# Performance work log

Hardware: AMD Instinct MI355X
Metric: run time of the kernel (lower is better)

The kernel has to match this reference:

```python
import jax, jax.numpy as jnp
import numpy as np

DIM = 1024
HEADS = 16
HEAD_DIM = DIM // HEADS
ROPE_BASE = 500000.0
SCALE = HEAD_DIM ** -0.5


def _rope_cos_sin(T, dtype=jnp.float32):
    inv_freq = 1.0 / (ROPE_BASE ** (jnp.arange(0, HEAD_DIM, 2, dtype=jnp.float32) / HEAD_DIM))
    t = jnp.arange(T, dtype=jnp.float32)
    freqs = t[:, None] * inv_freq[None, :]            # (T, hd/2)
    emb = jnp.concatenate([freqs, freqs], axis=-1)    # (T, hd)
    return jnp.cos(emb).astype(dtype), jnp.sin(emb).astype(dtype)


def _rotate_half(x):
    x1, x2 = jnp.split(x, 2, axis=-1)
    return jnp.concatenate([-x2, x1], axis=-1)


def _apply_rope(x, cos, sin):
    # x: (B,H,T,hd); cos/sin: (T,hd)
    return x * cos + _rotate_half(x) * sin


def setup_inputs() -> dict:
    key = jax.random.key(0)
    k1, k2, k3 = jax.random.split(key, 3)
    B, T = 4, 4096
    x = jax.random.normal(k1, (B, T, DIM), dtype=jnp.float32)
    W_qkv = jax.random.normal(k2, (DIM, 3 * DIM), dtype=jnp.float32) * (DIM ** -0.5)
    W_out = jax.random.normal(k3, (DIM, DIM), dtype=jnp.float32) * (DIM ** -0.5)
    return {"x": x, "W_qkv": W_qkv, "W_out": W_out}


def reference(x, W_qkv, W_out):
    B, T, D = x.shape
    H, hd = HEADS, HEAD_DIM
    qkv = (x @ W_qkv).reshape(B, T, 3, H, hd).transpose(2, 0, 3, 1, 4)  # (3,B,H,T,hd)
    q, k, v = qkv[0], qkv[1], qkv[2]
    cos, sin = _rope_cos_sin(T, q.dtype)
    q = _apply_rope(q, cos, sin)
    k = _apply_rope(k, cos, sin)
    # linear attention: elu+1 feature map
    q_feat = jax.nn.elu(q * SCALE) + 1.0
    k_feat = jax.nn.elu(k) + 1.0
    kv = jnp.einsum('bhtd,bhtv->bhdv', k_feat, v)      # (B,H,hd,hd)
    k_sum = k_feat.sum(axis=2)                          # (B,H,hd)
    denom = jnp.maximum(jnp.einsum('bhtd,bhd->bht', q_feat, k_sum), 1e-6)
    out = jnp.einsum('bhtd,bhdv->bhtv', q_feat, kv) / denom[..., None]
    out = out.transpose(0, 2, 1, 3).reshape(B, T, D)
    return out @ W_out
```

## Files before the change

### kernel.cpp

```cpp
#include <hip/hip_runtime.h>
#include <hip/hip_bf16.h>

typedef __bf16 bf16;
typedef bf16 bf16x4 __attribute__((ext_vector_type(4)));
typedef bf16 bf16x8 __attribute__((ext_vector_type(8)));
typedef float f32x4 __attribute__((ext_vector_type(4)));

#define GLD_LDS16(gptr, lptr) \
  __builtin_amdgcn_global_load_lds((const __attribute__((address_space(1))) unsigned int*)(gptr), \
                                   (__attribute__((address_space(3))) unsigned int*)(lptr), 16, 0, 0)

__global__ __launch_bounds__(256) void f32_to_bf16(const float* __restrict__ in,
                                                   bf16* __restrict__ out) {
  const size_t i = ((size_t)blockIdx.x * 256 + threadIdx.x) * 8;
  float4 a = *(const float4*)(in + i);
  float4 b = *(const float4*)(in + i + 4);
  bf16x8 o;
  o[0] = (bf16)a.x; o[1] = (bf16)a.y; o[2] = (bf16)a.z; o[3] = (bf16)a.w;
  o[4] = (bf16)b.x; o[5] = (bf16)b.y; o[6] = (bf16)b.z; o[7] = (bf16)b.w;
  *(bf16x8*)(out + i) = o;
}

__global__ __launch_bounds__(256) void transpose_f32_bf16(const float* __restrict__ in,
                                                          bf16* __restrict__ out,
                                                          int R, int C) {
  __shared__ float tile[32][33];
  const int bx = blockIdx.x * 32;
  const int by = blockIdx.y * 32;
  const int tx = threadIdx.x & 31;
  const int ty = threadIdx.x >> 5;
#pragma unroll
  for (int i = 0; i < 4; i++) {
    int r = by + ty + i * 8;
    tile[ty + i * 8][tx] = in[(size_t)r * C + bx + tx];
  }
  __syncthreads();
#pragma unroll
  for (int i = 0; i < 4; i++) {
    int r = bx + ty + i * 8;
    out[(size_t)r * R + by + tx] = (bf16)tile[tx][ty + i * 8];
  }
}

__device__ __forceinline__ void gemm_core(const bf16* __restrict__ A,
                                          const bf16* __restrict__ BT,
                                          int K, int m0, int n0,
                                          bf16* As, bf16* Bs,
                                          f32x4 acc[4][4]) {
  const int tid = threadIdx.x;
  const int lane = tid & 63;
  const int wave = tid >> 6;
  const int wm = wave & 1, wn = wave >> 1;

#pragma unroll
  for (int i = 0; i < 4; i++)
#pragma unroll
    for (int j = 0; j < 4; j++) acc[i][j] = f32x4{0.f, 0.f, 0.f, 0.f};

  const int srow = lane >> 3;
  const int pch = lane & 7;
  const int scol = (pch ^ srow) * 8;
  const int rbase = wave * 32;

  const bf16* Ag = A + (size_t)(m0 + rbase + srow) * K + scol;
  const bf16* Bg = BT + (size_t)(n0 + rbase + srow) * K + scol;
  bf16* Al = As + rbase * 64;
  bf16* Bl = Bs + rbase * 64;

  for (int k0 = 0; k0 < K; k0 += 64) {
#pragma unroll
    for (int i = 0; i < 4; i++) {
      GLD_LDS16(Ag + (size_t)i * 8 * K + k0, Al + i * 512);
      GLD_LDS16(Bg + (size_t)i * 8 * K + k0, Bl + i * 512);
    }
    __syncthreads();
    const int fr = lane & 15;
    const int sw = fr & 7;
#pragma unroll
    for (int kk = 0; kk < 64; kk += 32) {
      const int lc = (kk >> 3) + (lane >> 4);
      const int pc8 = (lc ^ sw) * 8;
      bf16x8 af[4], bfv[4];
#pragma unroll
      for (int mi = 0; mi < 4; mi++)
        af[mi] = *(const bf16x8*)(As + (wm * 64 + mi * 16 + fr) * 64 + pc8);
#pragma unroll
      for (int ni = 0; ni < 4; ni++)
        bfv[ni] = *(const bf16x8*)(Bs + (wn * 64 + ni * 16 + fr) * 64 + pc8);
#pragma unroll
      for (int mi = 0; mi < 4; mi++)
#pragma unroll
        for (int ni = 0; ni < 4; ni++)
          acc[mi][ni] = __builtin_amdgcn_mfma_f32_16x16x32_bf16(af[mi], bfv[ni], acc[mi][ni], 0, 0, 0);
    }
    __syncthreads();
  }
}

__global__ __launch_bounds__(256) void gemm_qkv_fused(const bf16* __restrict__ A,
                                                      const bf16* __restrict__ BT,
                                                      bf16* __restrict__ qfB,
                                                      bf16* __restrict__ kfB,
                                                      bf16* __restrict__ vfB) {
  __shared__ __attribute__((aligned(16))) bf16 As[128 * 64];
  __shared__ __attribute__((aligned(16))) bf16 Bs[128 * 64];
  const int K = 1024;
  const int m0 = blockIdx.y * 128, n0 = blockIdx.x * 128;

  f32x4 acc[4][4];
  gemm_core(A, BT, K, m0, n0, As, Bs, acc);

  const int lane = threadIdx.x & 63;
  const int wave = threadIdx.x >> 6;
  const int wm = wave & 1, wn = wave >> 1;
  const int cb = n0 + wn * 64;
  const int p = cb >> 10;
  const int hh = (cb & 1023) >> 6;
  const int fr15 = lane & 15;
  const int row00 = m0 + wm * 64 + ((lane >> 4) << 2);
  const int b = row00 >> 12;
  const size_t base0 = ((size_t)(b * 16 + hh)) * 4096 * 64;

  if (p == 2) {
#pragma unroll
    for (int mi = 0; mi < 4; mi++)
#pragma unroll
      for (int r = 0; r < 4; r++) {
        const int tloc = (row00 + mi * 16 + r) & 4095;
        bf16* dst = vfB + base0 + (size_t)tloc * 64;
#pragma unroll
        for (int ni = 0; ni < 4; ni++) dst[fr15 + ni * 16] = (bf16)acc[mi][ni][r];
      }
  } else {
    bf16* outp = (p == 0) ? qfB : kfB;
    const float scl = (p == 0) ? 0.125f : 1.0f;
    const float invf0 = (float)exp(-((double)fr15 / 32.0) * log(500000.0));
    const float invf1 = (float)exp(-((double)(fr15 + 16) / 32.0) * log(500000.0));
#pragma unroll
    for (int mi = 0; mi < 4; mi++)
#pragma unroll
      for (int r = 0; r < 4; r++) {
        const int tloc = (row00 + mi * 16 + r) & 4095;
        const float tf = (float)tloc;
        bf16* dst = outp + base0 + (size_t)tloc * 64;
#pragma unroll
        for (int ni = 0; ni < 2; ni++) {
          float x1 = acc[mi][ni][r], x2 = acc[mi][ni + 2][r];
          float sn, cs;
          sincosf(tf * (ni ? invf1 : invf0), &sn, &cs);
          float r1 = (x1 * cs - x2 * sn) * scl;
          float r2 = (x2 * cs + x1 * sn) * scl;
          dst[fr15 + ni * 16] = (bf16)(r1 > 0.f ? r1 + 1.f : __expf(r1));
          dst[fr15 + ni * 16 + 32] = (bf16)(r2 > 0.f ? r2 + 1.f : __expf(r2));
        }
      }
  }
}

__global__ __launch_bounds__(256) void gemm_bt_f32(const bf16* __restrict__ A,
                                                   const bf16* __restrict__ BT,
                                                   float* __restrict__ C,
                                                   int N, int K) {
  __shared__ __attribute__((aligned(16))) bf16 As[128 * 64];
  __shared__ __attribute__((aligned(16))) bf16 Bs[128 * 64];
  const int m0 = blockIdx.y * 128, n0 = blockIdx.x * 128;

  f32x4 acc[4][4];
  gemm_core(A, BT, K, m0, n0, As, Bs, acc);

  const int lane = threadIdx.x & 63;
  const int wave = threadIdx.x >> 6;
  const int wm = wave & 1, wn = wave >> 1;
  const int col0 = n0 + wn * 64 + (lane & 15);
  const int row00 = m0 + wm * 64 + ((lane >> 4) << 2);
#pragma unroll
  for (int mi = 0; mi < 4; mi++)
#pragma unroll
    for (int ni = 0; ni < 4; ni++)
#pragma unroll
      for (int r = 0; r < 4; r++)
        C[(size_t)(row00 + mi * 16 + r) * N + col0 + ni * 16] = acc[mi][ni][r];
}

__global__ __launch_bounds__(256) void attn_kv(const bf16* __restrict__ kfB,
                                               const bf16* __restrict__ vfB,
                                               float* __restrict__ kvg,
                                               float* __restrict__ ksumg) {
  const int bh = blockIdx.x;
  const int t0 = blockIdx.y * 256;
  __shared__ __attribute__((aligned(16))) float kfs[32][68];
  __shared__ __attribute__((aligned(16))) float vfs[32][68];
  const int tid = threadIdx.x;
  const int dq = tid & 15, g = tid >> 4;
  const int tl = tid >> 3, ch = (tid & 7) * 8;

  f32x4 acc[4];
#pragma unroll
  for (int r = 0; r < 4; r++) acc[r] = f32x4{0.f, 0.f, 0.f, 0.f};
  float ksa[4] = {0.f, 0.f, 0.f, 0.f};

  for (int sc = 0; sc < 8; sc++) {
    const size_t rowb = ((size_t)bh * 4096 + t0 + sc * 32 + tl) * 64 + ch;
    bf16x8 k8 = *(const bf16x8*)(kfB + rowb);
    bf16x8 v8 = *(const bf16x8*)(vfB + rowb);
    f32x4 ka, kb, va, vb;
#pragma unroll
    for (int j = 0; j < 4; j++) {
      ka[j] = (float)k8[j]; kb[j] = (float)k8[j + 4];
      va[j] = (float)v8[j]; vb[j] = (float)v8[j + 4];
    }
    *(f32x4*)&kfs[tl][ch] = ka;
    *(f32x4*)&kfs[tl][ch + 4] = kb;
    *(f32x4*)&vfs[tl][ch] = va;
    *(f32x4*)&vfs[tl][ch + 4] = vb;
    __syncthreads();

#pragma unroll 8
    for (int t = 0; t < 32; t++) {
      f32x4 kq = *(const f32x4*)&kfs[t][dq * 4];
      f32x4 vq = *(const f32x4*)&vfs[t][g * 4];
#pragma unroll
      for (int r = 0; r < 4; r++) {
#pragma unroll
        for (int c = 0; c < 4; c++) acc[r][c] += kq[r] * vq[c];
      }
      if (g == 0) {
#pragma unroll
        for (int r = 0; r < 4; r++) ksa[r] += kq[r];
      }
    }
    __syncthreads();
  }

#pragma unroll
  for (int r = 0; r < 4; r++)
#pragma unroll
    for (int c = 0; c < 4; c++)
      atomicAdd(&kvg[(size_t)bh * 4096 + (dq * 4 + r) * 64 + g * 4 + c], acc[r][c]);
  if (g == 0) {
#pragma unroll
    for (int r = 0; r < 4; r++) atomicAdd(&ksumg[bh * 64 + dq * 4 + r], ksa[r]);
  }
}

__global__ __launch_bounds__(256) void attn_out(const bf16* __restrict__ qfB,
                                                const float* __restrict__ kvg,
                                                const float* __restrict__ ksumg,
                                                bf16* __restrict__ attn) {
  const int bh = blockIdx.y;
  const int b = bh >> 4, h = bh & 15;
  const int t0 = blockIdx.x * 64;
  __shared__ __attribute__((aligned(16))) float qf[64][68];
  __shared__ __attribute__((aligned(16))) float kvs[64][64];
  __shared__ __attribute__((aligned(16))) float ksums[64];
  const int tid = threadIdx.x;

#pragma unroll
  for (int j = 0; j < 2; j++) {
    int chunk = tid + 256 * j;
    int tl = chunk >> 3, col = (chunk & 7) * 8;
    bf16x8 r = *(const bf16x8*)(qfB + ((size_t)bh * 4096 + t0 + tl) * 64 + col);
    f32x4 a, bb;
#pragma unroll
    for (int q = 0; q < 4; q++) { a[q] = (float)r[q]; bb[q] = (float)r[q + 4]; }
    *(f32x4*)&qf[tl][col] = a;
    *(f32x4*)&qf[tl][col + 4] = bb;
  }
#pragma unroll
  for (int j = 0; j < 4; j++) {
    int idx = tid + 256 * j;
    *(float4*)&kvs[idx >> 4][(idx & 15) * 4] = *(const float4*)&kvg[(size_t)bh * 4096 + idx * 4];
  }
  if (tid < 64) ksums[tid] = ksumg[bh * 64 + tid];
  __syncthreads();

  const int tr = tid >> 4, cc = tid & 15;
  f32x4 acc[4];
#pragma unroll
  for (int r = 0; r < 4; r++) acc[r] = f32x4{0.f, 0.f, 0.f, 0.f};
  f32x4 dn = f32x4{0.f, 0.f, 0.f, 0.f};

  for (int d2 = 0; d2 < 64; d2++) {
    f32x4 kv4 = *(const f32x4*)&kvs[d2][cc * 4];
    float ks = ksums[d2];
#pragma unroll
    for (int r = 0; r < 4; r++) {
      float qv = qf[tr * 4 + r][d2];
      acc[r] += qv * kv4;
      dn[r] += qv * ks;
    }
  }

#pragma unroll
  for (int r = 0; r < 4; r++) {
    const float rdn = 1.f / fmaxf(dn[r], 1e-6f);
    bf16x4 o;
#pragma unroll
    for (int c = 0; c < 4; c++) o[c] = (bf16)(acc[r][c] * rdn);
    *(bf16x4*)(attn + ((size_t)(b * 4096) + t0 + tr * 4 + r) * 1024 + h * 64 + cc * 4) = o;
  }
}

extern "C" void kernel_launch(void* const* d_in, const int* in_sizes, int n_in,
                              void* d_out, int out_size, void* d_ws, size_t ws_size,
                              hipStream_t stream) {
  if (ws_size < 177225728ULL) return;

  const float* x = (const float*)d_in[0];
  const float* Wqkv = (const float*)d_in[1];
  const float* Wout = (const float*)d_in[2];
  float* out = (float*)d_out;
  char* ws = (char*)d_ws;

  float* kvg = (float*)(ws);
  float* ksumg = (float*)(ws + 1048576);
  bf16* WqkvT = (bf16*)(ws + 1064960);
  bf16* WoutT = (bf16*)(ws + 7356416);
  bf16* attn = (bf16*)(ws + 9453568);
  bf16* qfB = (bf16*)(ws + 43008000);
  bf16* kfB = (bf16*)(ws + 76562432);
  bf16* vfB = (bf16*)(ws + 110116864);
  bf16* xB = (bf16*)(ws + 143671296);

  hipMemsetAsync(ws, 0, 1048576 + 16384, stream);

  f32_to_bf16<<<16777216 / (256 * 8), 256, 0, stream>>>(x, xB);
  transpose_f32_bf16<<<dim3(3072 / 32, 1024 / 32), 256, 0, stream>>>(Wqkv, WqkvT, 1024, 3072);
  transpose_f32_bf16<<<dim3(1024 / 32, 1024 / 32), 256, 0, stream>>>(Wout, WoutT, 1024, 1024);

  gemm_qkv_fused<<<dim3(3072 / 128, 16384 / 128), 256, 0, stream>>>(xB, WqkvT, qfB, kfB, vfB);

  attn_kv<<<dim3(64, 16), 256, 0, stream>>>(kfB, vfB, kvg, ksumg);
  attn_out<<<dim3(64, 64), 256, 0, stream>>>(qfB, kvg, ksumg, attn);

  gemm_bt_f32<<<dim3(1024 / 128, 16384 / 128), 256, 0, stream>>>(attn, WoutT, out, 1024, 1024);
}
```

Baseline: 430.9 us.

## Use 256x256 double-buffered GEMM with XCD tile swizzle and precomputed RoPE table

```diff
diff --git a/kernel.cpp b/kernel.cpp
--- a/kernel.cpp
+++ b/kernel.cpp
@@ -42,88 +42,189 @@
   }
 }
 
-__device__ __forceinline__ void gemm_core(const bf16* __restrict__ A,
-                                          const bf16* __restrict__ BT,
-                                          int K, int m0, int n0,
-                                          bf16* As, bf16* Bs,
-                                          f32x4 acc[4][4]) {
+__global__ __launch_bounds__(256) void rope_tab(float2* __restrict__ ctab) {
+  const int idx = blockIdx.x * 256 + threadIdx.x;
+  const int t = idx >> 5, f = idx & 31;
+  const float invf = (float)exp(-((double)f / 32.0) * log(500000.0));
+  float sn, cs;
+  sincosf((float)t * invf, &sn, &cs);
+  ctab[idx] = make_float2(cs, sn);
+}
+
+__device__ __forceinline__ void gemm256_core(const bf16* __restrict__ A,
+                                             const bf16* __restrict__ BT,
+                                             const int K, const int m0, const int n0,
+                                             bf16* __restrict__ As, bf16* __restrict__ Bs,
+                                             f32x4 acc[8][4]) {
   const int tid = threadIdx.x;
   const int lane = tid & 63;
-  const int wave = tid >> 6;
-  const int wm = wave & 1, wn = wave >> 1;
-
-#pragma unroll
-  for (int i = 0; i < 4; i++)
+  const int w = tid >> 6;
+  const int wm = w >> 2, wn = w & 3;
+
+#pragma unroll
+  for (int i = 0; i < 8; i++)
 #pragma unroll
     for (int j = 0; j < 4; j++) acc[i][j] = f32x4{0.f, 0.f, 0.f, 0.f};
 
-  const int srow = lane >> 3;
-  const int pch = lane & 7;
-  const int scol = (pch ^ srow) * 8;
-  const int rbase = wave * 32;
-
-  const bf16* Ag = A + (size_t)(m0 + rbase + srow) * K + scol;
-  const bf16* Bg = BT + (size_t)(n0 + rbase + srow) * K + scol;
-  bf16* Al = As + rbase * 64;
-  bf16* Bl = Bs + rbase * 64;
-
-  for (int k0 = 0; k0 < K; k0 += 64) {
-#pragma unroll
-    for (int i = 0; i < 4; i++) {
-      GLD_LDS16(Ag + (size_t)i * 8 * K + k0, Al + i * 512);
-      GLD_LDS16(Bg + (size_t)i * 8 * K + k0, Bl + i * 512);
-    }
-    __syncthreads();
-    const int fr = lane & 15;
-    const int sw = fr & 7;
-#pragma unroll
-    for (int kk = 0; kk < 64; kk += 32) {
-      const int lc = (kk >> 3) + (lane >> 4);
-      const int pc8 = (lc ^ sw) * 8;
-      bf16x8 af[4], bfv[4];
-#pragma unroll
-      for (int mi = 0; mi < 4; mi++)
-        af[mi] = *(const bf16x8*)(As + (wm * 64 + mi * 16 + fr) * 64 + pc8);
-#pragma unroll
-      for (int ni = 0; ni < 4; ni++)
-        bfv[ni] = *(const bf16x8*)(Bs + (wn * 64 + ni * 16 + fr) * 64 + pc8);
-#pragma unroll
-      for (int mi = 0; mi < 4; mi++)
-#pragma unroll
-        for (int ni = 0; ni < 4; ni++)
-          acc[mi][ni] = __builtin_amdgcn_mfma_f32_16x16x32_bf16(af[mi], bfv[ni], acc[mi][ni], 0, 0, 0);
-    }
-    __syncthreads();
-  }
-}
-
-__global__ __launch_bounds__(256) void gemm_qkv_fused(const bf16* __restrict__ A,
-                                                      const bf16* __restrict__ BT,
-                                                      bf16* __restrict__ qfB,
-                                                      bf16* __restrict__ kfB,
-                                                      bf16* __restrict__ vfB) {
-  __shared__ __attribute__((aligned(16))) bf16 As[128 * 64];
-  __shared__ __attribute__((aligned(16))) bf16 Bs[128 * 64];
+  const int rA = (w << 3) + (lane >> 3);
+  const int colS = (((lane & 7) ^ ((lane >> 3) & 7)) << 3);
+  const bf16* Ag = A + (size_t)(m0 + rA) * K + colS;
+  const bf16* Bg = BT + (size_t)(n0 + rA) * K + colS;
+  bf16* AsW = As + w * 512;
+  bf16* BsW = Bs + w * 512;
+
+#define STAGE2(G, L, h, k0)                                                        \
+  do {                                                                             \
+    GLD_LDS16((G) + (size_t)(h) * 128 * K + (k0), (L) + (h) * 8192);               \
+    GLD_LDS16((G) + (size_t)(h) * 128 * K + (size_t)64 * K + (k0),                 \
+              (L) + (h) * 8192 + 4096);                                            \
+  } while (0)
+
+  STAGE2(Ag, AsW, 0, 0);
+  STAGE2(Ag, AsW, 1, 0);
+  STAGE2(Bg, BsW, 0, 0);
+  STAGE2(Bg, BsW, 1, 0);
+  asm volatile("s_waitcnt vmcnt(0)" ::: "memory");
+  __builtin_amdgcn_s_barrier();
+
+  const int fr = lane & 15;
+  const int kq = lane >> 4;
+  const int swz = fr & 7;
+  const int pc0 = ((kq) ^ swz) << 3;
+  const int pc1 = ((4 + kq) ^ swz) << 3;
+
+  bf16x8 af[4][2], bv[4][2];
+  const int NT = K >> 6;
+
+  for (int kt = 0; kt < NT; ++kt) {
+    const int db = kt & 1;
+    const bf16* Ah = As + db * 16384 + wm * 8192;
+    const bf16* Bh = Bs + db * 16384 + (wn >> 1) * 8192;
+    const int cb = (wn & 1) * 64;
+    const int nk0 = (kt + 1) << 6;
+    const bool stg = (kt + 1 < NT);
+    bf16* AsN = AsW + (db ^ 1) * 16384;
+    bf16* BsN = BsW + (db ^ 1) * 16384;
+
+#pragma unroll
+    for (int mi = 0; mi < 4; mi++) {
+      af[mi][0] = *(const bf16x8*)(Ah + (mi * 16 + fr) * 64 + pc0);
+      af[mi][1] = *(const bf16x8*)(Ah + (mi * 16 + fr) * 64 + pc1);
+    }
+#pragma unroll
+    for (int ni = 0; ni < 2; ni++) {
+      bv[ni][0] = *(const bf16x8*)(Bh + (cb + ni * 16 + fr) * 64 + pc0);
+      bv[ni][1] = *(const bf16x8*)(Bh + (cb + ni * 16 + fr) * 64 + pc1);
+    }
+    if (stg) { STAGE2(Ag, AsN, 0, nk0); STAGE2(Ag, AsN, 1, nk0); }
+    __builtin_amdgcn_s_barrier();
+    asm volatile("s_waitcnt lgkmcnt(0)" ::: "memory");
+    __builtin_amdgcn_sched_barrier(0);
+    __builtin_amdgcn_s_setprio(1);
+#pragma unroll
+    for (int mi = 0; mi < 4; mi++)
+#pragma unroll
+      for (int ni = 0; ni < 2; ni++) {
+        acc[mi][ni] = __builtin_amdgcn_mfma_f32_16x16x32_bf16(af[mi][0], bv[ni][0], acc[mi][ni], 0, 0, 0);
+        acc[mi][ni] = __builtin_amdgcn_mfma_f32_16x16x32_bf16(af[mi][1], bv[ni][1], acc[mi][ni], 0, 0, 0);
+      }
+    __builtin_amdgcn_s_setprio(0);
+    __builtin_amdgcn_s_barrier();
+
+#pragma unroll
+    for (int ni = 2; ni < 4; ni++) {
+      bv[ni][0] = *(const bf16x8*)(Bh + (cb + ni * 16 + fr) * 64 + pc0);
+      bv[ni][1] = *(const bf16x8*)(Bh + (cb + ni * 16 + fr) * 64 + pc1);
+    }
+    if (stg) STAGE2(Bg, BsN, 0, nk0);
+    __builtin_amdgcn_s_barrier();
+    asm volatile("s_waitcnt lgkmcnt(0)" ::: "memory");
+    __builtin_amdgcn_sched_barrier(0);
+    __builtin_amdgcn_s_setprio(1);
+#pragma unroll
+    for (int mi = 0; mi < 4; mi++)
+#pragma unroll
+      for (int ni = 2; ni < 4; ni++) {
+        acc[mi][ni] = __builtin_amdgcn_mfma_f32_16x16x32_bf16(af[mi][0], bv[ni][0], acc[mi][ni], 0, 0, 0);
+        acc[mi][ni] = __builtin_amdgcn_mfma_f32_16x16x32_bf16(af[mi][1], bv[ni][1], acc[mi][ni], 0, 0, 0);
+      }
+    __builtin_amdgcn_s_setprio(0);
+    __builtin_amdgcn_s_barrier();
+
+#pragma unroll
+    for (int mi = 0; mi < 4; mi++) {
+      af[mi][0] = *(const bf16x8*)(Ah + (64 + mi * 16 + fr) * 64 + pc0);
+      af[mi][1] = *(const bf16x8*)(Ah + (64 + mi * 16 + fr) * 64 + pc1);
+    }
+    if (stg) STAGE2(Bg, BsN, 1, nk0);
+    __builtin_amdgcn_s_barrier();
+    asm volatile("s_waitcnt lgkmcnt(0)" ::: "memory");
+    __builtin_amdgcn_sched_barrier(0);
+    __builtin_amdgcn_s_setprio(1);
+#pragma unroll
+    for (int mi = 0; mi < 4; mi++)
+#pragma unroll
+      for (int ni = 2; ni < 4; ni++) {
+        acc[mi + 4][ni] = __builtin_amdgcn_mfma_f32_16x16x32_bf16(af[mi][0], bv[ni][0], acc[mi + 4][ni], 0, 0, 0);
+        acc[mi + 4][ni] = __builtin_amdgcn_mfma_f32_16x16x32_bf16(af[mi][1], bv[ni][1], acc[mi + 4][ni], 0, 0, 0);
+      }
+    __builtin_amdgcn_s_setprio(0);
+    __builtin_amdgcn_s_barrier();
+
+    __builtin_amdgcn_s_setprio(1);
+#pragma unroll
+    for (int mi = 0; mi < 4; mi++)
+#pragma unroll
+      for (int ni = 0; ni < 2; ni++) {
+        acc[mi + 4][ni] = __builtin_amdgcn_mfma_f32_16x16x32_bf16(af[mi][0], bv[ni][0], acc[mi + 4][ni], 0, 0, 0);
+        acc[mi + 4][ni] = __builtin_amdgcn_mfma_f32_16x16x32_bf16(af[mi][1], bv[ni][1], acc[mi + 4][ni], 0, 0, 0);
+      }
+    __builtin_amdgcn_s_setprio(0);
+    asm volatile("s_waitcnt vmcnt(0)" ::: "memory");
+    __builtin_amdgcn_s_barrier();
+  }
+#undef STAGE2
+}
+
+__device__ __forceinline__ void xcd_tile(int& m0, int& n0) {
+  const int gx = gridDim.x;
+  const int nwg = gx * gridDim.y;
+  const int orig = blockIdx.y * gx + blockIdx.x;
+  const int cpx = nwg >> 3;
+  const int swb = (orig & 7) * cpx + (orig >> 3);
+  m0 = (swb / gx) * 256;
+  n0 = (swb % gx) * 256;
+}
+
+__global__ __launch_bounds__(512, 2) void gemm_qkv_fused(const bf16* __restrict__ A,
+                                                         const bf16* __restrict__ BT,
+                                                         const float2* __restrict__ ctab,
+                                                         bf16* __restrict__ qfB,
+                                                         bf16* __restrict__ kfB,
+                                                         bf16* __restrict__ vfB) {
+  __shared__ __attribute__((aligned(16))) bf16 As[32768];
+  __shared__ __attribute__((aligned(16))) bf16 Bs[32768];
   const int K = 1024;
-  const int m0 = blockIdx.y * 128, n0 = blockIdx.x * 128;
-
-  f32x4 acc[4][4];
-  gemm_core(A, BT, K, m0, n0, As, Bs, acc);
+  int m0, n0;
+  xcd_tile(m0, n0);
+
+  f32x4 acc[8][4];
+  gemm256_core(A, BT, K, m0, n0, As, Bs, acc);
 
   const int lane = threadIdx.x & 63;
-  const int wave = threadIdx.x >> 6;
-  const int wm = wave & 1, wn = wave >> 1;
+  const int w = threadIdx.x >> 6;
+  const int wm = w >> 2, wn = w & 3;
+  const int fr15 = lane & 15;
   const int cb = n0 + wn * 64;
   const int p = cb >> 10;
   const int hh = (cb & 1023) >> 6;
-  const int fr15 = lane & 15;
-  const int row00 = m0 + wm * 64 + ((lane >> 4) << 2);
+  const int row00 = m0 + wm * 128 + ((lane >> 4) << 2);
   const int b = row00 >> 12;
   const size_t base0 = ((size_t)(b * 16 + hh)) * 4096 * 64;
 
   if (p == 2) {
 #pragma unroll
-    for (int mi = 0; mi < 4; mi++)
+    for (int mi = 0; mi < 8; mi++)
 #pragma unroll
       for (int r = 0; r < 4; r++) {
         const int tloc = (row00 + mi * 16 + r) & 4095;
@@ -134,22 +235,19 @@
   } else {
     bf16* outp = (p == 0) ? qfB : kfB;
     const float scl = (p == 0) ? 0.125f : 1.0f;
-    const float invf0 = (float)exp(-((double)fr15 / 32.0) * log(500000.0));
-    const float invf1 = (float)exp(-((double)(fr15 + 16) / 32.0) * log(500000.0));
-#pragma unroll
-    for (int mi = 0; mi < 4; mi++)
+#pragma unroll
+    for (int mi = 0; mi < 8; mi++)
 #pragma unroll
       for (int r = 0; r < 4; r++) {
         const int tloc = (row00 + mi * 16 + r) & 4095;
-        const float tf = (float)tloc;
+        const float2* ct = ctab + tloc * 32;
         bf16* dst = outp + base0 + (size_t)tloc * 64;
 #pragma unroll
         for (int ni = 0; ni < 2; ni++) {
-          float x1 = acc[mi][ni][r], x2 = acc[mi][ni + 2][r];
-          float sn, cs;
-          sincosf(tf * (ni ? invf1 : invf0), &sn, &cs);
-          float r1 = (x1 * cs - x2 * sn) * scl;
-          float r2 = (x2 * cs + x1 * sn) * scl;
+          const float2 cs2 = ct[fr15 + ni * 16];
+          const float x1 = acc[mi][ni][r], x2 = acc[mi][ni + 2][r];
+          const float r1 = (x1 * cs2.x - x2 * cs2.y) * scl;
+          const float r2 = (x2 * cs2.x + x1 * cs2.y) * scl;
           dst[fr15 + ni * 16] = (bf16)(r1 > 0.f ? r1 + 1.f : __expf(r1));
           dst[fr15 + ni * 16 + 32] = (bf16)(r2 > 0.f ? r2 + 1.f : __expf(r2));
         }
@@ -157,24 +255,25 @@
   }
 }
 
-__global__ __launch_bounds__(256) void gemm_bt_f32(const bf16* __restrict__ A,
-                                                   const bf16* __restrict__ BT,
-                                                   float* __restrict__ C,
-                                                   int N, int K) {
-  __shared__ __attribute__((aligned(16))) bf16 As[128 * 64];
-  __shared__ __attribute__((aligned(16))) bf16 Bs[128 * 64];
-  const int m0 = blockIdx.y * 128, n0 = blockIdx.x * 128;
-
-  f32x4 acc[4][4];
-  gemm_core(A, BT, K, m0, n0, As, Bs, acc);
+__global__ __launch_bounds__(512, 2) void gemm_bt_f32(const bf16* __restrict__ A,
+                                                      const bf16* __restrict__ BT,
+                                                      float* __restrict__ C,
+                                                      int N, int K) {
+  __shared__ __attribute__((aligned(16))) bf16 As[32768];
+  __shared__ __attribute__((aligned(16))) bf16 Bs[32768];
+  int m0, n0;
+  xcd_tile(m0, n0);
+
+  f32x4 acc[8][4];
+  gemm256_core(A, BT, K, m0, n0, As, Bs, acc);
 
   const int lane = threadIdx.x & 63;
-  const int wave = threadIdx.x >> 6;
-  const int wm = wave & 1, wn = wave >> 1;
+  const int w = threadIdx.x >> 6;
+  const int wm = w >> 2, wn = w & 3;
   const int col0 = n0 + wn * 64 + (lane & 15);
-  const int row00 = m0 + wm * 64 + ((lane >> 4) << 2);
-#pragma unroll
-  for (int mi = 0; mi < 4; mi++)
+  const int row00 = m0 + wm * 128 + ((lane >> 4) << 2);
+#pragma unroll
+  for (int mi = 0; mi < 8; mi++)
 #pragma unroll
     for (int ni = 0; ni < 4; ni++)
 #pragma unroll
@@ -317,6 +416,7 @@
   bf16* WqkvT = (bf16*)(ws + 1064960);
   bf16* WoutT = (bf16*)(ws + 7356416);
   bf16* attn = (bf16*)(ws + 9453568);
+  float2* ctab = (float2*)(ws + 9453568);
   bf16* qfB = (bf16*)(ws + 43008000);
   bf16* kfB = (bf16*)(ws + 76562432);
   bf16* vfB = (bf16*)(ws + 110116864);
@@ -324,14 +424,15 @@
 
   hipMemsetAsync(ws, 0, 1048576 + 16384, stream);
 
+  rope_tab<<<512, 256, 0, stream>>>(ctab);
   f32_to_bf16<<<16777216 / (256 * 8), 256, 0, stream>>>(x, xB);
   transpose_f32_bf16<<<dim3(3072 / 32, 1024 / 32), 256, 0, stream>>>(Wqkv, WqkvT, 1024, 3072);
   transpose_f32_bf16<<<dim3(1024 / 32, 1024 / 32), 256, 0, stream>>>(Wout, WoutT, 1024, 1024);
 
-  gemm_qkv_fused<<<dim3(3072 / 128, 16384 / 128), 256, 0, stream>>>(xB, WqkvT, qfB, kfB, vfB);
+  gemm_qkv_fused<<<dim3(3072 / 256, 16384 / 256), 512, 0, stream>>>(xB, WqkvT, ctab, qfB, kfB, vfB);
 
   attn_kv<<<dim3(64, 16), 256, 0, stream>>>(kfB, vfB, kvg, ksumg);
   attn_out<<<dim3(64, 64), 256, 0, stream>>>(qfB, kvg, ksumg, attn);
 
-  gemm_bt_f32<<<dim3(1024 / 128, 16384 / 128), 256, 0, stream>>>(attn, WoutT, out, 1024, 1024);
-}
+  gemm_bt_f32<<<dim3(1024 / 256, 16384 / 256), 512, 0, stream>>>(attn, WoutT, out, 1024, 1024);
+}
```

After: 385.9 us. 10.4% less time.
